# Kernel optimization log

Hardware: AMD Instinct MI355X
Metric: run time of the kernel (lower is better)

The kernel has to match this reference:

```python
import jax, jax.numpy as jnp
import numpy as np

ALPHA = 0.2  # LeakyReLU negative slope


def setup_inputs() -> dict:
    key = jax.random.key(0)
    k1, k2, k3 = jax.random.split(key, 3)
    B, N, F_in, F_out = 8, 2048, 128, 128
    x = jax.random.normal(k1, (B, N, F_in), dtype=jnp.float32)
    # nn.Linear weight: (out_features, in_features)
    W = jax.random.normal(k2, (F_out, F_in), dtype=jnp.float32) * (1.0 / np.sqrt(F_in))
    # attention vector a: (1, 2*out_features), xavier-uniform-like scale
    lim = np.sqrt(6.0 / (1 + 2 * F_out))
    a = jax.random.uniform(k3, (1, 2 * F_out), dtype=jnp.float32, minval=-lim, maxval=lim)
    return {"x": x, "W": W, "a": a}


def reference(x, W, a):
    # x: (B, N, F_in), W: (F_out, F_in), a: (1, 2*F_out)
    F_out = W.shape[0]
    h = jnp.einsum("bnf,of->bno", x, W)  # (B, N, F_out)
    # score_ij = leaky_relu(h_i . a[:F_out] + h_j . a[F_out:])
    # This is the math of cat([h_i, h_j]) * a summed over last dim,
    # WITHOUT materializing the (B,N,N,2F) concat tensor.
    a1 = a[0, :F_out]   # (F_out,)
    a2 = a[0, F_out:]   # (F_out,)
    si = h @ a1         # (B, N)  contribution from h_i
    sj = h @ a2         # (B, N)  contribution from h_j
    e = si[:, :, None] + sj[:, None, :]            # (B, N, N)
    e = jnp.where(e >= 0, e, ALPHA * e)            # leaky_relu
    attention = jax.nn.softmax(e, axis=-1)         # (B, N, N)
    # dropout is identity in eval mode
    output = jnp.einsum("bij,bjo->bio", attention, h)  # (B, N, F_out)
    return output
```

## Files before the change

### kernel.cpp

```cpp
#include <hip/hip_runtime.h>
#include <math.h>

#define BB 8
#define NN 2048
#define FF 128
#define LALPHA 0.2f
#define CH 16
#define NCH (NN / CH)

#define K1R 64
__global__ __launch_bounds__(256, 1)
void k1_h(const float* __restrict__ x, const float* __restrict__ W,
          const float* __restrict__ a, float* __restrict__ h,
          float* __restrict__ si, float* __restrict__ sj, int* __restrict__ cnt)
{
    __shared__ float Wt[FF * 132];
    const int t = threadIdx.x;
    const int row0 = blockIdx.x * K1R;

    if (blockIdx.x == 0)
        for (int kk = t; kk < BB * NCH; kk += 256) cnt[kk] = 0;

    for (int kk = t; kk < FF * FF; kk += 256) {
        int o = kk >> 7, f = kk & (FF - 1);
        Wt[f * 132 + o] = W[kk];
    }
    __syncthreads();

    const int tx = t & 15, ty = t >> 4;
    const int oq = tx << 3;
    const int rq = ty << 2;
    float acc[4][8];
#pragma unroll
    for (int r = 0; r < 4; ++r)
#pragma unroll
        for (int c = 0; c < 8; ++c) acc[r][c] = 0.f;

    for (int f0 = 0; f0 < FF; f0 += 4) {
        float4 xv[4];
#pragma unroll
        for (int r = 0; r < 4; ++r)
            xv[r] = *(const float4*)&x[(size_t)(row0 + rq + r) * FF + f0];
#pragma unroll
        for (int ff = 0; ff < 4; ++ff) {
            float4 w0 = *(const float4*)&Wt[(f0 + ff) * 132 + oq];
            float4 w1 = *(const float4*)&Wt[(f0 + ff) * 132 + oq + 4];
            const float wc[8] = {w0.x, w0.y, w0.z, w0.w, w1.x, w1.y, w1.z, w1.w};
#pragma unroll
            for (int r = 0; r < 4; ++r) {
                const float xr = (ff == 0) ? xv[r].x : (ff == 1) ? xv[r].y
                               : (ff == 2) ? xv[r].z : xv[r].w;
#pragma unroll
                for (int c = 0; c < 8; ++c)
                    acc[r][c] += xr * wc[c];
            }
        }
    }
#pragma unroll
    for (int r = 0; r < 4; ++r) {
        float* hp = &h[(size_t)(row0 + rq + r) * FF + oq];
        *(float4*)hp       = make_float4(acc[r][0], acc[r][1], acc[r][2], acc[r][3]);
        *(float4*)(hp + 4) = make_float4(acc[r][4], acc[r][5], acc[r][6], acc[r][7]);
    }
    const float4 a10 = *(const float4*)&a[oq];
    const float4 a11 = *(const float4*)&a[oq + 4];
    const float4 a20 = *(const float4*)&a[FF + oq];
    const float4 a21 = *(const float4*)&a[FF + oq + 4];
    const float a1v[8] = {a10.x, a10.y, a10.z, a10.w, a11.x, a11.y, a11.z, a11.w};
    const float a2v[8] = {a20.x, a20.y, a20.z, a20.w, a21.x, a21.y, a21.z, a21.w};
#pragma unroll
    for (int r = 0; r < 4; ++r) {
        float s1 = 0.f, s2 = 0.f;
#pragma unroll
        for (int c = 0; c < 8; ++c) { s1 += acc[r][c] * a1v[c]; s2 += acc[r][c] * a2v[c]; }
#pragma unroll
        for (int off = 8; off >= 1; off >>= 1) {
            s1 += __shfl_down(s1, off, 16);
            s2 += __shfl_down(s2, off, 16);
        }
        if (tx == 0) { si[row0 + rq + r] = s1; sj[row0 + rq + r] = s2; }
    }
}

__global__ __launch_bounds__(1024)
void k2_rank(const float* __restrict__ sj, float* __restrict__ keys, int* __restrict__ sidx,
             float* __restrict__ ew1, float* __restrict__ ew2)
{
    __shared__ float lk[NN];
    const int b = blockIdx.x >> 5;
    const int s = blockIdx.x & 31;
    const int t = threadIdx.x;
    for (int j = t; j < NN; j += 1024) lk[j] = sj[b * NN + j];
    __syncthreads();
    const int e = s * 64 + (t >> 4);
    const int slice = t & 15;
    const float ki = lk[e];
    const float4* lk4 = (const float4*)lk;
    int r = 0;
#pragma unroll 8
    for (int it = 0; it < 32; ++it) {
        int q = slice + (it << 4);
        float4 v = lk4[q];
        int j = q << 2;
        r += (v.x < ki || (v.x == ki && (j + 0) < e));
        r += (v.y < ki || (v.y == ki && (j + 1) < e));
        r += (v.z < ki || (v.z == ki && (j + 2) < e));
        r += (v.w < ki || (v.w == ki && (j + 3) < e));
    }
    r += __shfl_down(r, 8, 16);
    r += __shfl_down(r, 4, 16);
    r += __shfl_down(r, 2, 16);
    r += __shfl_down(r, 1, 16);
    if (slice == 0) {
        keys[b * NN + r] = ki;
        sidx[b * NN + r] = e;
        ew1[b * NN + r] = expf(ki);
        ew2[b * NN + r] = expf(LALPHA * ki);
    }
}

__global__ __launch_bounds__(128)
void k3a_csum(const float* __restrict__ h, const float* __restrict__ keys,
              const int* __restrict__ sidx, const float* __restrict__ si,
              const float* __restrict__ ew1, const float* __restrict__ ew2,
              float* __restrict__ csum1, float* __restrict__ csum2,
              float* __restrict__ ssum1, float* __restrict__ ssum2,
              int* __restrict__ cnt, int* __restrict__ brows)
{
    const int bid = blockIdx.x;
    const int b = bid >> 7, c = bid & (NCH - 1);
    const int o = threadIdx.x;
    const int m0 = c * CH;

    __shared__ float lw1[CH], lw2[CH];
    __shared__ int li[CH];
    __shared__ float bkey[NCH];
    if (o < CH) {
        lw1[o] = ew1[b * NN + m0 + o];
        lw2[o] = ew2[b * NN + m0 + o];
        li[o]  = sidx[b * NN + m0 + o];
    }
    bkey[o] = keys[b * NN + (o << 4)];
    __syncthreads();

    float r[CH];
#pragma unroll
    for (int m = 0; m < CH; ++m)
        r[m] = h[(size_t)(b * NN + li[m]) * FF + o];

    float a1 = 0.f, a2 = 0.f, s1 = 0.f, s2 = 0.f;
#pragma unroll
    for (int m = 0; m < CH; ++m) {
        float w1 = lw1[m], w2 = lw2[m];
        a1 += w1 * r[m]; a2 += w2 * r[m];
        s1 += w1;        s2 += w2;
    }
    csum1[(size_t)bid * FF + o] = a1;
    csum2[(size_t)bid * FF + o] = a2;
    if (o == 0) { ssum1[bid] = s1; ssum2[bid] = s2; }

    const int rl = o >> 3, slice = o & 7;
    const int i = m0 + rl;
    const float thr = -si[b * NN + i];
    int cc = 0;
#pragma unroll
    for (int k = 0; k < 16; ++k) {
        int c2 = slice * 16 + k;
        cc += (c2 >= 1) && (bkey[c2] < thr);
    }
    cc += __shfl_down(cc, 4, 8);
    cc += __shfl_down(cc, 2, 8);
    cc += __shfl_down(cc, 1, 8);
    if (slice == 0) {
        int pos = atomicAdd(&cnt[b * NCH + cc], 1);
        brows[(size_t)(b * NCH + cc) * NN + pos] = i;
    }
}

__global__ __launch_bounds__(256)
void k3se_emit(const float* __restrict__ h, const float* __restrict__ keys,
               const int* __restrict__ sidx, const float* __restrict__ si,
               const float* __restrict__ ew1, const float* __restrict__ ew2,
               const float* __restrict__ csum1, const float* __restrict__ csum2,
               const float* __restrict__ ssum1, const float* __restrict__ ssum2,
               const int* __restrict__ cnt, const int* __restrict__ brows,
               float* __restrict__ out)
{
    __shared__ float hs[CH][FF];
    __shared__ float S1pos[CH + 1][FF];
    __shared__ float P2pos[CH + 1][FF];
    __shared__ float lw1[CH], lw2[CH], lkey[CH];
    __shared__ float T1pos[CH + 1], T2pos[CH + 1];
    __shared__ float ls1[NCH], ls2[NCH];
    __shared__ float bp1[2][FF], bp2[2][FF];

    const int bid = blockIdx.x;
    const int b = bid >> 7, c = bid & (NCH - 1);
    const int t = threadIdx.x;
    const int o = t & 127, ht = t >> 7;
    const int m0 = c * CH;

    if (t < CH) {
        lkey[t] = keys[b * NN + m0 + t];
        lw1[t]  = ew1[b * NN + m0 + t];
        lw2[t]  = ew2[b * NN + m0 + t];
    }
    if (ht == 0) ls1[o] = ssum1[b * NCH + o];
    else         ls2[o] = ssum2[b * NCH + o];
    for (int kk = t; kk < CH * FF; kk += 256) {
        int m = kk >> 7, f = kk & 127;
        hs[m][f] = h[(size_t)(b * NN + sidx[b * NN + m0 + m]) * FF + f];
    }

    {
        const int c2lo = ht << 6, c2hi = c2lo + 64;
        float a1 = 0.f, a2 = 0.f;
        const int lo1 = (c + 1 > c2lo) ? c + 1 : c2lo;
#pragma unroll 8
        for (int c2 = lo1; c2 < c2hi; ++c2)
            a1 += csum1[(size_t)(b * NCH + c2) * FF + o];
        const int hi2 = (c < c2hi) ? c : c2hi;
#pragma unroll 8
        for (int c2 = c2lo; c2 < hi2; ++c2)
            a2 += csum2[(size_t)(b * NCH + c2) * FF + o];
        bp1[ht][o] = a1;
        bp2[ht][o] = a2;
    }
    __syncthreads();

    if (ht == 0) {
        float s = bp1[0][o] + bp1[1][o];
        S1pos[CH][o] = s;
#pragma unroll
        for (int m = CH - 1; m >= 0; --m) {
            s += lw1[m] * hs[m][o];
            S1pos[m][o] = s;
        }
        if (t < CH + 1) {
            float ts = 0.f;
#pragma unroll 8
            for (int c2 = c + 1; c2 < NCH; ++c2) ts += ls1[c2];
            for (int mm = CH - 1; mm >= t; --mm) ts += lw1[mm];
            T1pos[t] = ts;
        }
    } else {
        float s = bp2[0][o] + bp2[1][o];
        P2pos[0][o] = s;
#pragma unroll
        for (int m = 0; m < CH; ++m) {
            s += lw2[m] * hs[m][o];
            P2pos[m + 1][o] = s;
        }
        if (o < CH + 1) {
            float ts = 0.f;
#pragma unroll 8
            for (int c2 = 0; c2 < c; ++c2) ts += ls2[c2];
            for (int mm = 0; mm < o; ++mm) ts += lw2[mm];
            T2pos[o] = ts;
        }
    }
    __syncthreads();

    const int nrows = cnt[b * NCH + c];
    const int* br = brows + (size_t)(b * NCH + c) * NN;

    for (int r0 = 0; r0 < nrows; r0 += 2) {
        const int ri = r0 + ht;
        if (ri < nrows) {
            const int i = br[ri];
            const float siv = si[b * NN + i];
            const float thr = -siv;
            int rel = 0;
#pragma unroll
            for (int m = 0; m < CH; ++m) rel += (lkey[m] < thr);
            const float e1 = expf(siv), e2 = expf(LALPHA * siv);
            const float num = e1 * S1pos[rel][o] + e2 * P2pos[rel][o];
            const float den = e1 * T1pos[rel] + e2 * T2pos[rel];
            out[(size_t)(b * NN + i) * FF + o] = num / den;
        }
    }
}

extern "C" void kernel_launch(void* const* d_in, const int* in_sizes, int n_in,
                              void* d_out, int out_size, void* d_ws, size_t ws_size,
                              hipStream_t stream)
{
    const float* x = (const float*)d_in[0];
    const float* W = (const float*)d_in[1];
    const float* a = (const float*)d_in[2];
    float* out = (float*)d_out;

    float* ws = (float*)d_ws;
    float* h     = ws;
    float* si    = h + BB * NN * FF;
    float* sj    = si + BB * NN;
    float* keys  = sj + BB * NN;
    int*   sidx  = (int*)(keys + BB * NN);
    float* ew1   = (float*)(sidx + BB * NN);
    float* ew2   = ew1 + BB * NN;
    float* csum1 = ew2 + BB * NN;
    float* csum2 = csum1 + BB * NCH * FF;
    float* ssum1 = csum2 + BB * NCH * FF;
    float* ssum2 = ssum1 + BB * NCH;
    int*   cnt   = (int*)(ssum2 + BB * NCH);
    int*   brows = cnt + BB * NCH;

    hipLaunchKernelGGL(k1_h, dim3(BB * NN / K1R), dim3(256), 0, stream, x, W, a, h, si, sj, cnt);
    hipLaunchKernelGGL(k2_rank, dim3(BB * 32), dim3(1024), 0, stream, sj, keys, sidx, ew1, ew2);
    hipLaunchKernelGGL(k3a_csum, dim3(BB * NCH), dim3(128), 0, stream,
                       h, keys, sidx, si, ew1, ew2, csum1, csum2, ssum1, ssum2, cnt, brows);
    hipLaunchKernelGGL(k3se_emit, dim3(BB * NCH), dim3(256), 0, stream,
                       h, keys, sidx, si, ew1, ew2, csum1, csum2, ssum1, ssum2, cnt, brows, out);
}
```

Before: 57.32 us.

## Replace global row bucketing with per-block local bucketing over grouped chunks

Drops the global atomic bucket lists (cnt/brows) built in k3a_csum. The emit kernel now handles GC=4 consecutive chunks per block and scans all rows itself, bucketing them into shared-memory lists with LDS atomics. Running prefix sums are carried from one chunk to the next inside the block. This removes the global atomics, the large brows traffic and the cnt zeroing, but cuts the emit grid to a quarter of the blocks. Each local bucket is also capped at 256 rows, so a skewed key distribution would silently drop rows.

```diff
diff --git a/kernel.cpp b/kernel.cpp
--- a/kernel.cpp
+++ b/kernel.cpp
@@ -7,19 +7,18 @@
 #define LALPHA 0.2f
 #define CH 16
 #define NCH (NN / CH)
+#define GC 4
+#define NG (NCH / GC)
 
 #define K1R 64
 __global__ __launch_bounds__(256, 1)
 void k1_h(const float* __restrict__ x, const float* __restrict__ W,
           const float* __restrict__ a, float* __restrict__ h,
-          float* __restrict__ si, float* __restrict__ sj, int* __restrict__ cnt)
+          float* __restrict__ si, float* __restrict__ sj)
 {
     __shared__ float Wt[FF * 132];
     const int t = threadIdx.x;
     const int row0 = blockIdx.x * K1R;
-
-    if (blockIdx.x == 0)
-        for (int kk = t; kk < BB * NCH; kk += 256) cnt[kk] = 0;
 
     for (int kk = t; kk < FF * FF; kk += 256) {
         int o = kk >> 7, f = kk & (FF - 1);
@@ -120,12 +119,10 @@
 }
 
 __global__ __launch_bounds__(128)
-void k3a_csum(const float* __restrict__ h, const float* __restrict__ keys,
-              const int* __restrict__ sidx, const float* __restrict__ si,
+void k3a_csum(const float* __restrict__ h, const int* __restrict__ sidx,
               const float* __restrict__ ew1, const float* __restrict__ ew2,
               float* __restrict__ csum1, float* __restrict__ csum2,
-              float* __restrict__ ssum1, float* __restrict__ ssum2,
-              int* __restrict__ cnt, int* __restrict__ brows)
+              float* __restrict__ ssum1, float* __restrict__ ssum2)
 {
     const int bid = blockIdx.x;
     const int b = bid >> 7, c = bid & (NCH - 1);
@@ -134,13 +131,11 @@
 
     __shared__ float lw1[CH], lw2[CH];
     __shared__ int li[CH];
-    __shared__ float bkey[NCH];
     if (o < CH) {
         lw1[o] = ew1[b * NN + m0 + o];
         lw2[o] = ew2[b * NN + m0 + o];
         li[o]  = sidx[b * NN + m0 + o];
     }
-    bkey[o] = keys[b * NN + (o << 4)];
     __syncthreads();
 
     float r[CH];
@@ -158,125 +153,145 @@
     csum1[(size_t)bid * FF + o] = a1;
     csum2[(size_t)bid * FF + o] = a2;
     if (o == 0) { ssum1[bid] = s1; ssum2[bid] = s2; }
-
-    const int rl = o >> 3, slice = o & 7;
-    const int i = m0 + rl;
-    const float thr = -si[b * NN + i];
-    int cc = 0;
-#pragma unroll
-    for (int k = 0; k < 16; ++k) {
-        int c2 = slice * 16 + k;
-        cc += (c2 >= 1) && (bkey[c2] < thr);
-    }
-    cc += __shfl_down(cc, 4, 8);
-    cc += __shfl_down(cc, 2, 8);
-    cc += __shfl_down(cc, 1, 8);
-    if (slice == 0) {
-        int pos = atomicAdd(&cnt[b * NCH + cc], 1);
-        brows[(size_t)(b * NCH + cc) * NN + pos] = i;
-    }
 }
 
 __global__ __launch_bounds__(256)
-void k3se_emit(const float* __restrict__ h, const float* __restrict__ keys,
-               const int* __restrict__ sidx, const float* __restrict__ si,
-               const float* __restrict__ ew1, const float* __restrict__ ew2,
-               const float* __restrict__ csum1, const float* __restrict__ csum2,
-               const float* __restrict__ ssum1, const float* __restrict__ ssum2,
-               const int* __restrict__ cnt, const int* __restrict__ brows,
-               float* __restrict__ out)
+void k3fat(const float* __restrict__ h, const float* __restrict__ keys,
+           const int* __restrict__ sidx, const float* __restrict__ si,
+           const float* __restrict__ ew1, const float* __restrict__ ew2,
+           const float* __restrict__ csum1, const float* __restrict__ csum2,
+           const float* __restrict__ ssum1, const float* __restrict__ ssum2,
+           float* __restrict__ out)
 {
     __shared__ float hs[CH][FF];
     __shared__ float S1pos[CH + 1][FF];
     __shared__ float P2pos[CH + 1][FF];
+    __shared__ float bS1[FF], bP2[FF];
     __shared__ float lw1[CH], lw2[CH], lkey[CH];
     __shared__ float T1pos[CH + 1], T2pos[CH + 1];
     __shared__ float ls1[NCH], ls2[NCH];
     __shared__ float bp1[2][FF], bp2[2][FF];
+    __shared__ float bk[5];
+    __shared__ float tb1[GC], tb2[GC];
+    __shared__ int lcnt[GC];
+    __shared__ int lrows[GC][256];
 
     const int bid = blockIdx.x;
-    const int b = bid >> 7, c = bid & (NCH - 1);
+    const int b = bid >> 5, g = bid & (NG - 1);
     const int t = threadIdx.x;
     const int o = t & 127, ht = t >> 7;
-    const int m0 = c * CH;
-
-    if (t < CH) {
-        lkey[t] = keys[b * NN + m0 + t];
-        lw1[t]  = ew1[b * NN + m0 + t];
-        lw2[t]  = ew2[b * NN + m0 + t];
-    }
+    const int c0 = g * GC;
+
     if (ht == 0) ls1[o] = ssum1[b * NCH + o];
     else         ls2[o] = ssum2[b * NCH + o];
-    for (int kk = t; kk < CH * FF; kk += 256) {
-        int m = kk >> 7, f = kk & 127;
-        hs[m][f] = h[(size_t)(b * NN + sidx[b * NN + m0 + m]) * FF + f];
+    if (t < GC) lcnt[t] = 0;
+    if (t < 5) {
+        int idx = (c0 + t) * CH;
+        bk[t] = (idx < NN) ? keys[b * NN + idx] : 0.f;
+    }
+    __syncthreads();
+
+    {
+        const float bk0 = bk[0], bk1 = bk[1], bk2 = bk[2], bk3 = bk[3], bk4 = bk[4];
+        for (int k = 0; k < 8; ++k) {
+            int i = (k << 8) + t;
+            float thr = -si[b * NN + i];
+            bool ge = (g == 0) || (bk0 < thr);
+            bool lt = (g == NG - 1) || !(bk4 < thr);
+            if (ge && lt) {
+                int cc = (bk1 < thr) + (bk2 < thr) + (bk3 < thr);
+                int pos = atomicAdd(&lcnt[cc], 1);
+                if (pos < 256) lrows[cc][pos] = i;
+            }
+        }
     }
 
     {
         const int c2lo = ht << 6, c2hi = c2lo + 64;
         float a1 = 0.f, a2 = 0.f;
-        const int lo1 = (c + 1 > c2lo) ? c + 1 : c2lo;
+        const int lo1 = (c0 + 1 > c2lo) ? c0 + 1 : c2lo;
 #pragma unroll 8
         for (int c2 = lo1; c2 < c2hi; ++c2)
             a1 += csum1[(size_t)(b * NCH + c2) * FF + o];
-        const int hi2 = (c < c2hi) ? c : c2hi;
+        const int hi2 = (c0 < c2hi) ? c0 : c2hi;
 #pragma unroll 8
         for (int c2 = c2lo; c2 < hi2; ++c2)
             a2 += csum2[(size_t)(b * NCH + c2) * FF + o];
         bp1[ht][o] = a1;
         bp2[ht][o] = a2;
     }
-    __syncthreads();
-
-    if (ht == 0) {
-        float s = bp1[0][o] + bp1[1][o];
-        S1pos[CH][o] = s;
-#pragma unroll
-        for (int m = CH - 1; m >= 0; --m) {
-            s += lw1[m] * hs[m][o];
-            S1pos[m][o] = s;
-        }
-        if (t < CH + 1) {
-            float ts = 0.f;
-#pragma unroll 8
-            for (int c2 = c + 1; c2 < NCH; ++c2) ts += ls1[c2];
-            for (int mm = CH - 1; mm >= t; --mm) ts += lw1[mm];
-            T1pos[t] = ts;
-        }
-    } else {
-        float s = bp2[0][o] + bp2[1][o];
-        P2pos[0][o] = s;
-#pragma unroll
-        for (int m = 0; m < CH; ++m) {
-            s += lw2[m] * hs[m][o];
-            P2pos[m + 1][o] = s;
-        }
-        if (o < CH + 1) {
-            float ts = 0.f;
-#pragma unroll 8
-            for (int c2 = 0; c2 < c; ++c2) ts += ls2[c2];
-            for (int mm = 0; mm < o; ++mm) ts += lw2[mm];
-            T2pos[o] = ts;
-        }
-    }
-    __syncthreads();
-
-    const int nrows = cnt[b * NCH + c];
-    const int* br = brows + (size_t)(b * NCH + c) * NN;
-
-    for (int r0 = 0; r0 < nrows; r0 += 2) {
-        const int ri = r0 + ht;
-        if (ri < nrows) {
-            const int i = br[ri];
-            const float siv = si[b * NN + i];
-            const float thr = -siv;
-            int rel = 0;
-#pragma unroll
-            for (int m = 0; m < CH; ++m) rel += (lkey[m] < thr);
-            const float e1 = expf(siv), e2 = expf(LALPHA * siv);
-            const float num = e1 * S1pos[rel][o] + e2 * P2pos[rel][o];
-            const float den = e1 * T1pos[rel] + e2 * T2pos[rel];
-            out[(size_t)(b * NN + i) * FF + o] = num / den;
+    if (t < GC) {
+        float s = 0.f;
+        for (int c2 = c0 + t + 1; c2 < NCH; ++c2) s += ls1[c2];
+        tb1[t] = s;
+    } else if (t < 2 * GC) {
+        const int cc = t - GC;
+        float s = 0.f;
+        for (int c2 = 0; c2 < c0 + cc; ++c2) s += ls2[c2];
+        tb2[cc] = s;
+    }
+    __syncthreads();
+    if (ht == 0) bS1[o] = bp1[0][o] + bp1[1][o];
+    else         bP2[o] = bp2[0][o] + bp2[1][o];
+
+    for (int cc = 0; cc < GC; ++cc) {
+        const int c = c0 + cc;
+        const int m0 = c * CH;
+        __syncthreads();
+        if (t < CH) {
+            lkey[t] = keys[b * NN + m0 + t];
+            lw1[t]  = ew1[b * NN + m0 + t];
+            lw2[t]  = ew2[b * NN + m0 + t];
+        }
+        for (int kk = t; kk < CH * FF; kk += 256) {
+            int m = kk >> 7, f = kk & 127;
+            hs[m][f] = h[(size_t)(b * NN + sidx[b * NN + m0 + m]) * FF + f];
+        }
+        __syncthreads();
+
+        if (ht == 0) {
+            float s = bS1[o];
+            S1pos[CH][o] = s;
+#pragma unroll
+            for (int m = CH - 1; m >= 0; --m) { s += lw1[m] * hs[m][o]; S1pos[m][o] = s; }
+            if (t < CH + 1) {
+                float ts = tb1[cc];
+                for (int mm = CH - 1; mm >= t; --mm) ts += lw1[mm];
+                T1pos[t] = ts;
+            }
+        } else {
+            float s = bP2[o];
+            P2pos[0][o] = s;
+#pragma unroll
+            for (int m = 0; m < CH; ++m) { s += lw2[m] * hs[m][o]; P2pos[m + 1][o] = s; }
+            if (o < CH + 1) {
+                float ts = tb2[cc];
+                for (int mm = 0; mm < o; ++mm) ts += lw2[mm];
+                T2pos[o] = ts;
+            }
+        }
+        __syncthreads();
+
+        int nrows = lcnt[cc]; if (nrows > 256) nrows = 256;
+        for (int r0 = 0; r0 < nrows; r0 += 2) {
+            const int ri = r0 + ht;
+            if (ri < nrows) {
+                const int i = lrows[cc][ri];
+                const float siv = si[b * NN + i];
+                const float thr = -siv;
+                int rel = 0;
+#pragma unroll
+                for (int m = 0; m < CH; ++m) rel += (lkey[m] < thr);
+                const float e1 = expf(siv), e2 = expf(LALPHA * siv);
+                const float num = e1 * S1pos[rel][o] + e2 * P2pos[rel][o];
+                const float den = e1 * T1pos[rel] + e2 * T2pos[rel];
+                out[(size_t)(b * NN + i) * FF + o] = num / den;
+            }
+        }
+
+        if (cc < GC - 1) {
+            if (ht == 0) bS1[o] -= csum1[(size_t)(b * NCH + c + 1) * FF + o];
+            else         bP2[o] = P2pos[CH][o];
         }
     }
 }
@@ -302,13 +317,11 @@
     float* csum2 = csum1 + BB * NCH * FF;
     float* ssum1 = csum2 + BB * NCH * FF;
     float* ssum2 = ssum1 + BB * NCH;
-    int*   cnt   = (int*)(ssum2 + BB * NCH);
-    int*   brows = cnt + BB * NCH;
-
-    hipLaunchKernelGGL(k1_h, dim3(BB * NN / K1R), dim3(256), 0, stream, x, W, a, h, si, sj, cnt);
+
+    hipLaunchKernelGGL(k1_h, dim3(BB * NN / K1R), dim3(256), 0, stream, x, W, a, h, si, sj);
     hipLaunchKernelGGL(k2_rank, dim3(BB * 32), dim3(1024), 0, stream, sj, keys, sidx, ew1, ew2);
     hipLaunchKernelGGL(k3a_csum, dim3(BB * NCH), dim3(128), 0, stream,
-                       h, keys, sidx, si, ew1, ew2, csum1, csum2, ssum1, ssum2, cnt, brows);
-    hipLaunchKernelGGL(k3se_emit, dim3(BB * NCH), dim3(256), 0, stream,
-                       h, keys, sidx, si, ew1, ew2, csum1, csum2, ssum1, ssum2, cnt, brows, out);
-}
+                       h, sidx, ew1, ew2, csum1, csum2, ssum1, ssum2);
+    hipLaunchKernelGGL(k3fat, dim3(BB * NG), dim3(256), 0, stream,
+                       h, keys, sidx, si, ew1, ew2, csum1, csum2, ssum1, ssum2, out);
+}
```

Result: slower. 77.90 us (+35.9%).
